# Optimization experiments

Measured on AMD Instinct MI355X. Metric: run time of the kernel, lower is better.

The kernel has to match this reference:

```python
import jax, jax.numpy as jnp
import numpy as np

B, S, D_MODEL = 2, 4096, 2048
N_IDX_HEADS, D_HEAD = 4, 64


def setup_inputs() -> dict:
    key = jax.random.key(0)
    k1, k2, k3 = jax.random.split(key, 3)
    h = jax.random.normal(k1, (B, S, D_MODEL), dtype=jnp.float32)
    # torch Linear weights: [out_features, in_features]
    Wq = jax.random.normal(k2, (N_IDX_HEADS * D_HEAD, D_MODEL), dtype=jnp.float32) * (D_MODEL ** -0.5)
    Wk = jax.random.normal(k3, (D_HEAD, D_MODEL), dtype=jnp.float32) * (D_MODEL ** -0.5)
    w = jnp.ones((N_IDX_HEADS,), dtype=jnp.float32)
    return {"h": h, "Wq": Wq, "Wk": Wk, "w": w}


def reference(h, Wq, Wk, w):
    batch, seq, _ = h.shape
    # q: [B, T, H, Dh]; k: [B, S, Dh]
    q = (h @ Wq.T).reshape(batch, seq, N_IDX_HEADS, D_HEAD)
    k = h @ Wk.T
    # scores: [B, T, H, S]
    scores = jax.nn.relu(jnp.einsum('bthd,bsd->bths', q, k))
    # head-weighted sum -> I: [B, T, S]
    I = jnp.einsum('bths,h->bts', scores, w)
    return I
```

## Files before the change

kernel.cpp:

```cpp
#include <hip/hip_runtime.h>

typedef __attribute__((ext_vector_type(8))) short bf16x8;
typedef __attribute__((ext_vector_type(4))) float f32x4;
typedef __attribute__((ext_vector_type(8))) unsigned short us8;

#define K_DIM 2048
#define QK_N  320
#define SEQ   4096
#define BK    64
#define NCHUNK 32
#define NHALF  160
#define BM     64
#define BCHUNK 20480

__device__ __forceinline__ unsigned short f2bf(float f) {
    unsigned int u = __builtin_bit_cast(unsigned int, f);
    u += 0x7FFFu + ((u >> 16) & 1u);
    return (unsigned short)(u >> 16);
}

__device__ __forceinline__ void gld_lds16(const void* g, void* l) {
    __builtin_amdgcn_global_load_lds(
        (const __attribute__((address_space(1))) void*)g,
        (__attribute__((address_space(3))) void*)l,
        16, 0, 0);
}

__global__ void cvt_w_swz(const float* __restrict__ Wq,
                          const float* __restrict__ Wk,
                          unsigned short* __restrict__ ws) {
    int id = blockIdx.x * 256 + threadIdx.x;
    int c  = id >> 8;
    int k8 = id & 255;
    int k0 = k8 * 8;
    const float* src = (c < 256) ? (Wq + (size_t)c * K_DIM + k0)
                                 : (Wk + (size_t)(c - 256) * K_DIM + k0);
    float4 v0 = *reinterpret_cast<const float4*>(src);
    float4 v1 = *reinterpret_cast<const float4*>(src + 4);
    us8 o;
    o[0] = f2bf(v0.x); o[1] = f2bf(v0.y); o[2] = f2bf(v0.z); o[3] = f2bf(v0.w);
    o[4] = f2bf(v1.x); o[5] = f2bf(v1.y); o[6] = f2bf(v1.z); o[7] = f2bf(v1.w);
    int half = (c >= NHALF) ? 1 : 0;
    int cc   = c - half * NHALF;
    int kc = k0 / BK;
    int u  = (k0 % BK) >> 3;
    size_t byteoff = (size_t)half * (NCHUNK * (size_t)BCHUNK)
                   + (size_t)kc * BCHUNK + ((size_t)(u * NHALF + cc) * 16);
    *reinterpret_cast<us8*>((char*)ws + byteoff) = o;
}

__global__ __launch_bounds__(512, 2) void proj_gemm(
    const float* __restrict__ A,
    const unsigned short* __restrict__ Wsz,
    unsigned short* __restrict__ C)
{
    __shared__ unsigned short Asm[2][BM * BK];
    __shared__ unsigned short Bsm[2][BCHUNK / 2];

    const int tid  = threadIdx.x;
    const int lane = tid & 63;
    const int wid  = tid >> 6;
    const int rg   = wid >> 1;
    const int cg   = wid & 1;
    const int mrow0 = blockIdx.y * BM;
    const int half  = blockIdx.x;
    const int lr = lane & 15, lg = lane >> 4;

    const int ar = tid >> 3;
    const int au = tid & 7;
    const float* a_src = A + (size_t)(mrow0 + ar) * K_DIM + au * 8;
    const int a_dst_off = ((au << 6) + ar) << 4;

    const char* wsrc = (const char*)Wsz + (size_t)half * (NCHUNK * (size_t)BCHUNK)
                     + wid * 1024 + lane * 16;

    f32x4 acc[5];
#pragma unroll
    for (int j = 0; j < 5; ++j) acc[j] = (f32x4)0.f;

    auto stageB = [&](int kc, int buf) {
        const char* s = wsrc + (size_t)kc * BCHUNK;
        char* d = (char*)&Bsm[buf][0] + wid * 1024 + lane * 16;
        gld_lds16(s, d);
        gld_lds16(s + 8192, d + 8192);
        if (wid < 4) gld_lds16(s + 16384, d + 16384);
    };
    auto loadA = [&](int kc, float4& f0, float4& f1) {
        const float* p = a_src + (size_t)kc * BK;
        f0 = *reinterpret_cast<const float4*>(p);
        f1 = *reinterpret_cast<const float4*>(p + 4);
    };
    auto writeA = [&](float4 f0, float4 f1, int buf) {
        us8 o;
        o[0] = f2bf(f0.x); o[1] = f2bf(f0.y); o[2] = f2bf(f0.z); o[3] = f2bf(f0.w);
        o[4] = f2bf(f1.x); o[5] = f2bf(f1.y); o[6] = f2bf(f1.z); o[7] = f2bf(f1.w);
        *reinterpret_cast<us8*>((char*)&Asm[buf][0] + a_dst_off) = o;
    };
    auto compute = [&](int buf) {
        const char* ab = (const char*)&Asm[buf][0];
        const char* bb = (const char*)&Bsm[buf][0];
#pragma unroll
        for (int ks = 0; ks < 2; ++ks) {
            const int u = ks * 4 + lg;
            bf16x8 a = *reinterpret_cast<const bf16x8*>(
                ab + (((u << 6) + rg * 16 + lr) << 4));
            const char* bu = bb + (size_t)u * (NHALF * 16);
#pragma unroll
            for (int j = 0; j < 5; ++j) {
                bf16x8 b = *reinterpret_cast<const bf16x8*>(
                    bu + ((cg * 80 + j * 16 + lr) << 4));
                acc[j] = __builtin_amdgcn_mfma_f32_16x16x32_bf16(a, b, acc[j], 0, 0, 0);
            }
        }
    };

#define WAIT_BAR(N) do { \
        asm volatile("s_waitcnt vmcnt(" #N ") lgkmcnt(0)" ::: "memory"); \
        __builtin_amdgcn_s_barrier(); \
    } while (0)

    float4 r0a, r0b;
    float4 r1a, r1b;

    stageB(0, 0);
    loadA(0, r0a, r0b);
    asm volatile("s_waitcnt vmcnt(0)" ::: "memory");
    writeA(r0a, r0b, 0);
    loadA(1, r1a, r1b);
    asm volatile("s_waitcnt lgkmcnt(0)" ::: "memory");
    __builtin_amdgcn_s_barrier();

    for (int t = 0; t < NCHUNK; t += 2) {
        stageB(t + 1, 1);
        {
            int kc = (t + 2 < NCHUNK) ? t + 2 : NCHUNK - 1;
            loadA(kc, r0a, r0b);
        }
        compute(0);
        writeA(r1a, r1b, 1);
        WAIT_BAR(2);
        const int u = t + 1;
        if (u < NCHUNK - 1) {
            stageB(u + 1, 0);
            int kc = (u + 2 < NCHUNK) ? u + 2 : NCHUNK - 1;
            loadA(kc, r1a, r1b);
        }
        compute(1);
        if (u < NCHUNK - 1) {
            writeA(r0a, r0b, 0);
            WAIT_BAR(2);
        }
    }
#undef WAIT_BAR

    const int crow = mrow0 + rg * 16 + lg * 4;
    const int ccol = half * NHALF + cg * 80 + lr;
#pragma unroll
    for (int j = 0; j < 5; ++j)
#pragma unroll
        for (int r = 0; r < 4; ++r)
            C[(size_t)(crow + r) * QK_N + ccol + j * 16] = f2bf(acc[j][r]);
}

__global__ __launch_bounds__(256) void scores_kernel(
    const unsigned short* __restrict__ QK,
    const float* __restrict__ w,
    float* __restrict__ out)
{
    const int lane = threadIdx.x & 63;
    const int wid  = threadIdx.x >> 6;
    const int b  = blockIdx.z;
    const int t0 = blockIdx.y * 128 + (wid >> 1) * 64;
    const int s0 = blockIdx.x * 128 + (wid & 1) * 64;

    const int lr = lane & 15;
    const int lk = (lane >> 4) * 8;
    const int lg = lane >> 4;

    const unsigned short* Qb = QK + (size_t)b * SEQ * QK_N;
    const unsigned short* Kb = Qb + 256;

    float wv[4] = { w[0], w[1], w[2], w[3] };

    f32x4 fin[4][4];
#pragma unroll
    for (int i = 0; i < 4; ++i)
#pragma unroll
        for (int j = 0; j < 4; ++j) fin[i][j] = (f32x4)0.f;

    const unsigned short* qp = Qb + (size_t)(t0 + lr) * QK_N + lk;
    const unsigned short* kp = Kb + (size_t)(s0 + lr) * QK_N + lk;

#pragma unroll
    for (int h = 0; h < 4; ++h) {
        f32x4 acc[4][4];
#pragma unroll
        for (int i = 0; i < 4; ++i)
#pragma unroll
            for (int j = 0; j < 4; ++j) acc[i][j] = (f32x4)0.f;

#pragma unroll
        for (int ks = 0; ks < 2; ++ks) {
            bf16x8 qf[4], kf[4];
#pragma unroll
            for (int i = 0; i < 4; ++i)
                qf[i] = *reinterpret_cast<const bf16x8*>(
                    qp + (size_t)i * 16 * QK_N + h * 64 + ks * 32);
#pragma unroll
            for (int j = 0; j < 4; ++j)
                kf[j] = *reinterpret_cast<const bf16x8*>(
                    kp + (size_t)j * 16 * QK_N + ks * 32);
#pragma unroll
            for (int i = 0; i < 4; ++i)
#pragma unroll
                for (int j = 0; j < 4; ++j)
                    acc[i][j] = __builtin_amdgcn_mfma_f32_16x16x32_bf16(kf[j], qf[i], acc[i][j], 0, 0, 0);
        }
#pragma unroll
        for (int i = 0; i < 4; ++i)
#pragma unroll
            for (int j = 0; j < 4; ++j)
#pragma unroll
                for (int r = 0; r < 4; ++r)
                    fin[i][j][r] += wv[h] * fmaxf(acc[i][j][r], 0.f);
    }

    float* ob = out + (size_t)b * SEQ * SEQ;
#pragma unroll
    for (int i = 0; i < 4; ++i) {
        const size_t rbase = (size_t)(t0 + i * 16 + lr) * SEQ + s0 + lg * 4;
#pragma unroll
        for (int j = 0; j < 4; ++j) {
            float4 v;
            v.x = fin[i][j][0]; v.y = fin[i][j][1];
            v.z = fin[i][j][2]; v.w = fin[i][j][3];
            *reinterpret_cast<float4*>(&ob[rbase + j * 16]) = v;
        }
    }
}

extern "C" void kernel_launch(void* const* d_in, const int* in_sizes, int n_in,
                              void* d_out, int out_size, void* d_ws, size_t ws_size,
                              hipStream_t stream) {
    const float* h  = (const float*)d_in[0];
    const float* Wq = (const float*)d_in[1];
    const float* Wk = (const float*)d_in[2];
    const float* w  = (const float*)d_in[3];
    float* out = (float*)d_out;

    unsigned short* W_swz = (unsigned short*)d_ws;
    unsigned short* QKb   = (unsigned short*)((char*)d_ws + 2 * (size_t)NCHUNK * BCHUNK);

    cvt_w_swz<<<320, 256, 0, stream>>>(Wq, Wk, W_swz);
    proj_gemm<<<dim3(2, 128), 512, 0, stream>>>(h, W_swz, QKb);
    scores_kernel<<<dim3(32, 32, 2), 256, 0, stream>>>(QKb, w, out);
}
```

Before: 111.6 us.

## Replace LDS-staged double-buffered projection GEMM with direct global-load MFMA loop

The projection GEMM drops LDS staging, barriers and double buffering. Each wave now loads its A fragment (fp32 converted to bf16) and its B fragments straight from global memory into registers. The block shrinks to 256 threads covering 32 rows, and the grid doubles to 512 blocks for more parallelism. This removes barrier and LDS overhead but loses data sharing within a block, so the same global data is re-read by multiple waves and latency hiding depends on occupancy and the cache.

```diff
diff --git a/kernel.cpp b/kernel.cpp
--- a/kernel.cpp
+++ b/kernel.cpp
@@ -10,20 +10,12 @@
 #define BK    64
 #define NCHUNK 32
 #define NHALF  160
-#define BM     64
 #define BCHUNK 20480
 
 __device__ __forceinline__ unsigned short f2bf(float f) {
     unsigned int u = __builtin_bit_cast(unsigned int, f);
     u += 0x7FFFu + ((u >> 16) & 1u);
     return (unsigned short)(u >> 16);
-}
-
-__device__ __forceinline__ void gld_lds16(const void* g, void* l) {
-    __builtin_amdgcn_global_load_lds(
-        (const __attribute__((address_space(1))) void*)g,
-        (__attribute__((address_space(3))) void*)l,
-        16, 0, 0);
 }
 
 __global__ void cvt_w_swz(const float* __restrict__ Wq,
@@ -49,111 +41,53 @@
     *reinterpret_cast<us8*>((char*)ws + byteoff) = o;
 }
 
-__global__ __launch_bounds__(512, 2) void proj_gemm(
+__global__ __launch_bounds__(256) void proj_gemm(
     const float* __restrict__ A,
     const unsigned short* __restrict__ Wsz,
     unsigned short* __restrict__ C)
 {
-    __shared__ unsigned short Asm[2][BM * BK];
-    __shared__ unsigned short Bsm[2][BCHUNK / 2];
-
     const int tid  = threadIdx.x;
     const int lane = tid & 63;
     const int wid  = tid >> 6;
     const int rg   = wid >> 1;
     const int cg   = wid & 1;
-    const int mrow0 = blockIdx.y * BM;
-    const int half  = blockIdx.x;
+    const int half = blockIdx.x;
+    const int row0 = blockIdx.y * 32 + rg * 16;
     const int lr = lane & 15, lg = lane >> 4;
 
-    const int ar = tid >> 3;
-    const int au = tid & 7;
-    const float* a_src = A + (size_t)(mrow0 + ar) * K_DIM + au * 8;
-    const int a_dst_off = ((au << 6) + ar) << 4;
-
-    const char* wsrc = (const char*)Wsz + (size_t)half * (NCHUNK * (size_t)BCHUNK)
-                     + wid * 1024 + lane * 16;
+    const float* ap = A + (size_t)(row0 + lr) * K_DIM + lg * 8;
+    const char* wbase = (const char*)Wsz + (size_t)half * (NCHUNK * (size_t)BCHUNK)
+                      + ((cg * 80 + lr) << 4);
 
     f32x4 acc[5];
 #pragma unroll
     for (int j = 0; j < 5; ++j) acc[j] = (f32x4)0.f;
 
-    auto stageB = [&](int kc, int buf) {
-        const char* s = wsrc + (size_t)kc * BCHUNK;
-        char* d = (char*)&Bsm[buf][0] + wid * 1024 + lane * 16;
-        gld_lds16(s, d);
-        gld_lds16(s + 8192, d + 8192);
-        if (wid < 4) gld_lds16(s + 16384, d + 16384);
-    };
-    auto loadA = [&](int kc, float4& f0, float4& f1) {
-        const float* p = a_src + (size_t)kc * BK;
-        f0 = *reinterpret_cast<const float4*>(p);
-        f1 = *reinterpret_cast<const float4*>(p + 4);
-    };
-    auto writeA = [&](float4 f0, float4 f1, int buf) {
-        us8 o;
-        o[0] = f2bf(f0.x); o[1] = f2bf(f0.y); o[2] = f2bf(f0.z); o[3] = f2bf(f0.w);
-        o[4] = f2bf(f1.x); o[5] = f2bf(f1.y); o[6] = f2bf(f1.z); o[7] = f2bf(f1.w);
-        *reinterpret_cast<us8*>((char*)&Asm[buf][0] + a_dst_off) = o;
-    };
-    auto compute = [&](int buf) {
-        const char* ab = (const char*)&Asm[buf][0];
-        const char* bb = (const char*)&Bsm[buf][0];
-#pragma unroll
-        for (int ks = 0; ks < 2; ++ks) {
-            const int u = ks * 4 + lg;
-            bf16x8 a = *reinterpret_cast<const bf16x8*>(
-                ab + (((u << 6) + rg * 16 + lr) << 4));
-            const char* bu = bb + (size_t)u * (NHALF * 16);
-#pragma unroll
-            for (int j = 0; j < 5; ++j) {
-                bf16x8 b = *reinterpret_cast<const bf16x8*>(
-                    bu + ((cg * 80 + j * 16 + lr) << 4));
-                acc[j] = __builtin_amdgcn_mfma_f32_16x16x32_bf16(a, b, acc[j], 0, 0, 0);
-            }
-        }
-    };
+#pragma unroll 2
+    for (int t = 0; t < 64; ++t) {
+        const char* bu = wbase + (size_t)(t >> 1) * BCHUNK
+                       + (size_t)(((t & 1) * 4 + lg) * NHALF) * 16;
+        bf16x8 b0 = *reinterpret_cast<const bf16x8*>(bu);
+        bf16x8 b1 = *reinterpret_cast<const bf16x8*>(bu + 256);
+        bf16x8 b2 = *reinterpret_cast<const bf16x8*>(bu + 512);
+        bf16x8 b3 = *reinterpret_cast<const bf16x8*>(bu + 768);
+        bf16x8 b4 = *reinterpret_cast<const bf16x8*>(bu + 1024);
+        const float* p = ap + t * 32;
+        float4 x = *reinterpret_cast<const float4*>(p);
+        float4 y = *reinterpret_cast<const float4*>(p + 4);
+        bf16x8 a;
+        a[0] = (short)f2bf(x.x); a[1] = (short)f2bf(x.y);
+        a[2] = (short)f2bf(x.z); a[3] = (short)f2bf(x.w);
+        a[4] = (short)f2bf(y.x); a[5] = (short)f2bf(y.y);
+        a[6] = (short)f2bf(y.z); a[7] = (short)f2bf(y.w);
+        acc[0] = __builtin_amdgcn_mfma_f32_16x16x32_bf16(a, b0, acc[0], 0, 0, 0);
+        acc[1] = __builtin_amdgcn_mfma_f32_16x16x32_bf16(a, b1, acc[1], 0, 0, 0);
+        acc[2] = __builtin_amdgcn_mfma_f32_16x16x32_bf16(a, b2, acc[2], 0, 0, 0);
+        acc[3] = __builtin_amdgcn_mfma_f32_16x16x32_bf16(a, b3, acc[3], 0, 0, 0);
+        acc[4] = __builtin_amdgcn_mfma_f32_16x16x32_bf16(a, b4, acc[4], 0, 0, 0);
+    }
 
-#define WAIT_BAR(N) do { \
-        asm volatile("s_waitcnt vmcnt(" #N ") lgkmcnt(0)" ::: "memory"); \
-        __builtin_amdgcn_s_barrier(); \
-    } while (0)
-
-    float4 r0a, r0b;
-    float4 r1a, r1b;
-
-    stageB(0, 0);
-    loadA(0, r0a, r0b);
-    asm volatile("s_waitcnt vmcnt(0)" ::: "memory");
-    writeA(r0a, r0b, 0);
-    loadA(1, r1a, r1b);
-    asm volatile("s_waitcnt lgkmcnt(0)" ::: "memory");
-    __builtin_amdgcn_s_barrier();
-
-    for (int t = 0; t < NCHUNK; t += 2) {
-        stageB(t + 1, 1);
-        {
-            int kc = (t + 2 < NCHUNK) ? t + 2 : NCHUNK - 1;
-            loadA(kc, r0a, r0b);
-        }
-        compute(0);
-        writeA(r1a, r1b, 1);
-        WAIT_BAR(2);
-        const int u = t + 1;
-        if (u < NCHUNK - 1) {
-            stageB(u + 1, 0);
-            int kc = (u + 2 < NCHUNK) ? u + 2 : NCHUNK - 1;
-            loadA(kc, r1a, r1b);
-        }
-        compute(1);
-        if (u < NCHUNK - 1) {
-            writeA(r0a, r0b, 0);
-            WAIT_BAR(2);
-        }
-    }
-#undef WAIT_BAR
-
-    const int crow = mrow0 + rg * 16 + lg * 4;
+    const int crow = row0 + lg * 4;
     const int ccol = half * NHALF + cg * 80 + lr;
 #pragma unroll
     for (int j = 0; j < 5; ++j)
@@ -252,6 +186,6 @@
     unsigned short* QKb   = (unsigned short*)((char*)d_ws + 2 * (size_t)NCHUNK * BCHUNK);
 
     cvt_w_swz<<<320, 256, 0, stream>>>(Wq, Wk, W_swz);
-    proj_gemm<<<dim3(2, 128), 512, 0, stream>>>(h, W_swz, QKb);
+    proj_gemm<<<dim3(2, 256), 256, 0, stream>>>(h, W_swz, QKb);
     scores_kernel<<<dim3(32, 32, 2), 256, 0, stream>>>(QKb, w, out);
 }
```

Measured after the change: 124.3 us. 11.4% more time.
